# Optimization experiments

Hardware: AMD Instinct MI355X
Metric: run time of the kernel (lower is better)

Reference implementation:

```python
import jax, jax.numpy as jnp
import numpy as np

WIN = 7
NUM_HEADS = 4
HEAD_DIM = 32  # 128 / 4


def _relative_position_index(win=WIN):
    coords = np.stack(np.meshgrid(np.arange(win), np.arange(win), indexing='ij'))  # [2,w,w]
    coords = coords.reshape(2, -1)  # [2, w*w]
    rel = coords[:, :, None] - coords[:, None, :]  # [2, ws, ws]
    rel = rel.transpose(1, 2, 0)  # [ws, ws, 2]
    idx = (rel[..., 0] + win - 1) * (2 * win - 1) + (rel[..., 1] + win - 1)
    return jnp.asarray(idx, dtype=jnp.int32)  # [49, 49]


def setup_inputs() -> dict:
    key = jax.random.key(0)
    ks = jax.random.split(key, 6)
    B, S, D = 4096, WIN * WIN, 128
    nW = 64  # windows per image
    return {
        'hidden_states': jax.random.normal(ks[0], (B, S, D), dtype=jnp.float32),
        'attention_mask': jnp.zeros((nW, S, S), dtype=jnp.float32),
        'Wq': jax.random.normal(ks[1], (D, D), dtype=jnp.float32) * 0.02,
        'bq': jnp.zeros((D,), dtype=jnp.float32),
        'Wk': jax.random.normal(ks[2], (D, D), dtype=jnp.float32) * 0.02,
        'bk': jnp.zeros((D,), dtype=jnp.float32),
        'Wv': jax.random.normal(ks[3], (D, D), dtype=jnp.float32) * 0.02,
        'bv': jnp.zeros((D,), dtype=jnp.float32),
        'bias_table': jax.random.normal(ks[4], ((2 * WIN - 1) ** 2, NUM_HEADS), dtype=jnp.float32) * 0.02,
    }


def reference(hidden_states, attention_mask, Wq, bq, Wk, bk, Wv, bv, bias_table):
    B, S, D = hidden_states.shape
    H, Dh = NUM_HEADS, HEAD_DIM

    def heads(x):  # [B,S,D] -> [B,H,S,Dh]
        return x.reshape(B, S, H, Dh).transpose(0, 2, 1, 3)

    q = heads(hidden_states @ Wq + bq)
    k = heads(hidden_states @ Wk + bk)
    v = heads(hidden_states @ Wv + bv)

    scores = jnp.einsum('bhqd,bhkd->bhqk', q, k) / np.sqrt(Dh).astype(np.float32)

    idx = _relative_position_index()  # [S,S] int32 constant
    rel_bias = bias_table[idx]  # [S,S,H]
    scores = scores + rel_bias.transpose(2, 0, 1)[None]  # [B,H,S,S]

    nW = attention_mask.shape[0]
    scores = scores.reshape(B // nW, nW, H, S, S) + attention_mask[None, :, None]
    scores = scores.reshape(B, H, S, S)

    probs = jax.nn.softmax(scores, axis=-1)
    ctx = jnp.einsum('bhqk,bhkd->bhqd', probs, v)
    return ctx.transpose(0, 2, 1, 3).reshape(B, S, D)
```

## Files before the change

kernel.cpp:

```cpp
#include <hip/hip_runtime.h>
#include <hip/hip_bf16.h>

#define S49 49
#define D128 128
#define NH 4

typedef __attribute__((ext_vector_type(8))) short short8;
typedef __attribute__((ext_vector_type(4))) float f32x4;

__device__ __forceinline__ unsigned short f2b(float x){
  unsigned u = __builtin_bit_cast(unsigned, x);
  return (unsigned short)((u + 0x7fffu + ((u>>16)&1u)) >> 16);
}
__device__ __forceinline__ unsigned pk2(float a, float b){
  __hip_bfloat162 h = __float22bfloat162_rn(float2{a, b});
  unsigned u; __builtin_memcpy(&u, &h, 4);
  return u;
}
__device__ __forceinline__ int swz256i(int row, int col){
  return row*128 + ((((col>>3) ^ (row&15)) << 3) | (col&7));
}

__global__ void prep_wt(const float* __restrict__ Wq, const float* __restrict__ Wk,
                        const float* __restrict__ Wv, unsigned short* __restrict__ wt){
  int e = blockIdx.x*256 + threadIdx.x;
  if (e >= 3*128*128) return;
  int mat = e >> 14, rem = e & 16383, n = rem >> 7, k = rem & 127;
  const float* W = (mat==0) ? Wq : ((mat==1) ? Wk : Wv);
  wt[e] = f2b(W[k*128 + n]);
}

__global__ void prep_comb(const float* __restrict__ mask, const float* __restrict__ bt,
                          float4* __restrict__ comb4, int nW){
  int e = blockIdx.x*256 + threadIdx.x;
  if (e >= nW*NH*S49*16) return;
  int s = e & 15; int nt = s >> 2, lg = s & 3;
  int t = e >> 4;
  int i = t % S49; t /= S49;
  int h = t & (NH-1); int w = t / NH;
  const float* mrow = mask + ((size_t)w*S49 + i)*S49;
  int ri = i/7, ci = i - ri*7;
  const float L2E = 1.4426950408889634f;
  float v[4];
  #pragma unroll
  for (int r = 0; r < 4; ++r){
    int j = nt*16 + lg*4 + r;
    if (j < S49){
      int rj = j/7, cj = j - rj*7;
      int idx = (ri - rj + 6)*13 + (ci - cj + 6);
      v[r] = (mrow[j] + bt[idx*NH + h]) * L2E;
    } else v[r] = -1e30f;
  }
  float4 o; o.x = v[0]; o.y = v[1]; o.z = v[2]; o.w = v[3];
  comb4[e] = o;
}

__global__ __launch_bounds__(512, 6) void swin_attn(
    const float* __restrict__ hs,
    const float* __restrict__ bq, const float* __restrict__ bk,
    const float* __restrict__ bv,
    const float4* __restrict__ comb4,
    const unsigned short* __restrict__ wt, float* __restrict__ out, int nW){

  __shared__ __align__(16) unsigned short lds[26880];
  unsigned short* hs_s = lds;
  unsigned short* q_s  = lds + 6272;
  unsigned short* k_s  = lds + 12544;
  unsigned short* vt_s = lds + 18816;
  unsigned short* pext = lds + 25984;

  const int b = blockIdx.x;
  const int tid = threadIdx.x;
  const int wave = tid >> 6, lane = tid & 63;
  const int lg = lane >> 4, ln = lane & 15;
  unsigned short* pp = (wave < 7) ? (hs_s + wave*896) : pext;

  const float* hsb = hs + (size_t)b * (S49*D128);
  #pragma unroll
  for (int it = 0; it < 4; ++it) {
    int u = tid + it*512;
    if (u < S49*32) {
      int row = u >> 5, c = u & 31;
      float4 f = *(const float4*)(hsb + row*128 + c*4);
      uint2 o; o.x = pk2(f.x, f.y); o.y = pk2(f.z, f.w);
      *(uint2*)&hs_s[swz256i(row, c*4)] = o;
    }
  }
  if (tid < 128) {
    uint2 z2 = {0u,0u};
    *(uint2*)&vt_s[tid*56 + 48] = z2;
    *(uint2*)&vt_s[tid*56 + 52] = z2;
  }
  __syncthreads();

  const int w = b % nW;
  const int rt = wave & 3, hp = wave >> 2;
  const int mbw = (rt<3) ? rt*16 : 33;

  {
    const int ntb = wave*16;
    #pragma unroll 1
    for (int mat = 0; mat < 3; ++mat) {
      short8 a[4];
      #pragma unroll
      for (int ks = 0; ks < 4; ++ks)
        a[ks] = *(const short8*)&wt[(mat<<14) + (ntb+ln)*128 + ks*32 + lg*8];
      const float* bp = (mat==0) ? bq : ((mat==1) ? bk : bv);
      float4 bias = *(const float4*)&bp[ntb + 4*lg];
      #pragma unroll
      for (int mt = 0; mt < 4; ++mt) {
        const int mb = (mt<3) ? mt*16 : 33;
        short8 bh[4];
        #pragma unroll
        for (int ks = 0; ks < 4; ++ks)
          bh[ks] = *(const short8*)&hs_s[swz256i(mb+ln, ks*32 + lg*8)];
        f32x4 acc = {0.f,0.f,0.f,0.f};
        #pragma unroll
        for (int ks = 0; ks < 4; ++ks)
          acc = __builtin_amdgcn_mfma_f32_16x16x32_bf16(a[ks], bh[ks], acc, 0,0,0);
        const int m = mb + ln;
        const int nb = ntb + 4*lg;
        if (mat == 0) {
          uint2 o; o.x = pk2(acc[0]+bias.x, acc[1]+bias.y);
                   o.y = pk2(acc[2]+bias.z, acc[3]+bias.w);
          *(uint2*)&q_s[swz256i(m, nb)] = o;
        } else if (mat == 1) {
          uint2 o; o.x = pk2(acc[0]+bias.x, acc[1]+bias.y);
                   o.y = pk2(acc[2]+bias.z, acc[3]+bias.w);
          *(uint2*)&k_s[swz256i(m, nb)] = o;
        } else {
          vt_s[(nb+0)*56 + m] = f2b(acc[0]+bias.x);
          vt_s[(nb+1)*56 + m] = f2b(acc[1]+bias.y);
          vt_s[(nb+2)*56 + m] = f2b(acc[2]+bias.z);
          vt_s[(nb+3)*56 + m] = f2b(acc[3]+bias.w);
        }
      }
    }
  }
  __syncthreads();

  const float C1 = 0.17677669529663687f * 1.4426950408889634f;
  const short8 z8 = {0,0,0,0,0,0,0,0};

  #pragma unroll
  for (int hh = 0; hh < 2; ++hh) {
    const int h = hp*2 + hh;
    float4 cb[4];
    #pragma unroll
    for (int nt = 0; nt < 4; ++nt)
      cb[nt] = comb4[((size_t)((w*NH + h)*S49) + mbw + ln)*16 + nt*4 + lg];

    short8 aq = *(const short8*)&q_s[swz256i(mbw+ln, h*32 + lg*8)];
    short8 kb[4];
    #pragma unroll
    for (int nt = 0; nt < 4; ++nt)
      kb[nt] = *(const short8*)&k_s[swz256i(nt*16+ln, h*32 + lg*8)];
    if (ln != 0) kb[3] = z8;
    f32x4 st[4];
    __builtin_amdgcn_s_setprio(1);
    #pragma unroll
    for (int nt = 0; nt < 4; ++nt) {
      f32x4 z = {0.f,0.f,0.f,0.f};
      st[nt] = __builtin_amdgcn_mfma_f32_16x16x32_bf16(kb[nt], aq, z, 0,0,0);
    }
    __builtin_amdgcn_s_setprio(0);

    float e[4][4], psum[4];
    #pragma unroll
    for (int nt = 0; nt < 4; ++nt) {
      float cbv[4] = {cb[nt].x, cb[nt].y, cb[nt].z, cb[nt].w};
      #pragma unroll
      for (int r = 0; r < 4; ++r)
        e[nt][r] = __builtin_amdgcn_exp2f(fmaf(st[nt][r], C1, cbv[r]));
      psum[nt] = (e[nt][0] + e[nt][1]) + (e[nt][2] + e[nt][3]);
    }
    float sum = (psum[0] + psum[1]) + (psum[2] + psum[3]);
    sum += __shfl_xor(sum, 16, 64);
    sum += __shfl_xor(sum, 32, 64);
    const float inv = __builtin_amdgcn_rcpf(sum);

    #pragma unroll
    for (int nt = 0; nt < 4; ++nt) {
      #pragma unroll
      for (int rp = 0; rp < 2; ++rp) {
        if (nt < 3 || lg < 2) {
          unsigned u = pk2(e[nt][2*rp]*inv, e[nt][2*rp+1]*inv);
          *(unsigned*)&pp[ln*56 + nt*16 + lg*4 + 2*rp] = u;
        }
      }
    }

    short8 ap0 = *(const short8*)&pp[ln*56 + lg*8];
    short8 ap1 = z8;
    if (lg < 3) ap1 = *(const short8*)&pp[ln*56 + 32 + lg*8];
    #pragma unroll
    for (int nt = 0; nt < 2; ++nt) {
      const int vr = h*32 + nt*16 + ln;
      short8 bv0 = *(const short8*)&vt_s[vr*56 + lg*8];
      short8 bv1 = z8;
      if (lg < 3) bv1 = *(const short8*)&vt_s[vr*56 + 32 + lg*8];
      f32x4 acc = {0.f,0.f,0.f,0.f};
      __builtin_amdgcn_s_setprio(1);
      acc = __builtin_amdgcn_mfma_f32_16x16x32_bf16(ap0, bv0, acc, 0,0,0);
      acc = __builtin_amdgcn_mfma_f32_16x16x32_bf16(ap1, bv1, acc, 0,0,0);
      __builtin_amdgcn_s_setprio(0);
      const int mr = mbw + 4*lg;
      #pragma unroll
      for (int r = 0; r < 4; ++r)
        out[((size_t)b*S49 + mr + r)*D128 + vr] = acc[r];
    }
  }
}

extern "C" void kernel_launch(void* const* d_in, const int* in_sizes, int n_in,
                              void* d_out, int out_size, void* d_ws, size_t ws_size,
                              hipStream_t stream){
  const float* hs  = (const float*)d_in[0];
  const float* msk = (const float*)d_in[1];
  const float* Wq  = (const float*)d_in[2];
  const float* bq  = (const float*)d_in[3];
  const float* Wk  = (const float*)d_in[4];
  const float* bk  = (const float*)d_in[5];
  const float* Wv  = (const float*)d_in[6];
  const float* bv  = (const float*)d_in[7];
  const float* bt  = (const float*)d_in[8];
  unsigned short* wt = (unsigned short*)d_ws;
  float4* comb4 = (float4*)((char*)d_ws + 98304);
  float* out = (float*)d_out;
  const int B  = in_sizes[0] / (S49*D128);
  const int nW = in_sizes[1] / (S49*S49);
  prep_wt<<<dim3((3*128*128 + 255)/256), dim3(256), 0, stream>>>(Wq, Wk, Wv, wt);
  prep_comb<<<dim3((nW*NH*S49*16 + 255)/256), dim3(256), 0, stream>>>(msk, bt, comb4, nW);
  swin_attn<<<dim3(B), dim3(512), 0, stream>>>(hs, bq, bk, bv, comb4, wt, out, nW);
}
```

Measured before the change: 109.2 us.

## Permute key order so softmax probabilities feed the PV MFMA from registers

Keys are reordered through a lane-to-row mapping, krow, and the combined mask/bias table is permuted to match. The QK^T MFMA output then already sits in the A-operand layout the PV MFMA expects, so the probabilities are packed in registers instead of written to LDS and read back. This removes an LDS store/load round trip and shrinks shared memory. The V-transpose stride also changes from 56 to 58 to cut bank conflicts. The risks are that 16-byte LDS reads at a 58-element stride are not 16-byte aligned, and that padded key rows now read past k_s into other LDS data, relying only on the -1e30 bias to mask them.

```diff
diff --git a/kernel.cpp b/kernel.cpp
--- a/kernel.cpp
+++ b/kernel.cpp
@@ -4,8 +4,10 @@
 #define S49 49
 #define D128 128
 #define NH 4
+#define VTS 58
 
 typedef __attribute__((ext_vector_type(8))) short short8;
+typedef __attribute__((ext_vector_type(4))) unsigned uint4v;
 typedef __attribute__((ext_vector_type(4))) float f32x4;
 
 __device__ __forceinline__ unsigned short f2b(float x){
@@ -19,6 +21,9 @@
 }
 __device__ __forceinline__ int swz256i(int row, int col){
   return row*128 + ((((col>>3) ^ (row&15)) << 3) | (col&7));
+}
+__device__ __forceinline__ int krow(int nt, int ln){
+  return 8*(ln>>2) + (ln&3) + 4*(nt&1) + 32*(nt>>1);
 }
 
 __global__ void prep_wt(const float* __restrict__ Wq, const float* __restrict__ Wk,
@@ -44,7 +49,7 @@
   float v[4];
   #pragma unroll
   for (int r = 0; r < 4; ++r){
-    int j = nt*16 + lg*4 + r;
+    int j = 8*lg + 4*(nt&1) + 32*(nt>>1) + r;
     if (j < S49){
       int rj = j/7, cj = j - rj*7;
       int idx = (ri - rj + 6)*13 + (ci - cj + 6);
@@ -62,18 +67,16 @@
     const float4* __restrict__ comb4,
     const unsigned short* __restrict__ wt, float* __restrict__ out, int nW){
 
-  __shared__ __align__(16) unsigned short lds[26880];
+  __shared__ __align__(16) unsigned short lds[26240];
   unsigned short* hs_s = lds;
   unsigned short* q_s  = lds + 6272;
   unsigned short* k_s  = lds + 12544;
   unsigned short* vt_s = lds + 18816;
-  unsigned short* pext = lds + 25984;
 
   const int b = blockIdx.x;
   const int tid = threadIdx.x;
   const int wave = tid >> 6, lane = tid & 63;
   const int lg = lane >> 4, ln = lane & 15;
-  unsigned short* pp = (wave < 7) ? (hs_s + wave*896) : pext;
 
   const float* hsb = hs + (size_t)b * (S49*D128);
   #pragma unroll
@@ -86,10 +89,13 @@
       *(uint2*)&hs_s[swz256i(row, c*4)] = o;
     }
   }
-  if (tid < 128) {
-    uint2 z2 = {0u,0u};
-    *(uint2*)&vt_s[tid*56 + 48] = z2;
-    *(uint2*)&vt_s[tid*56 + 52] = z2;
+  #pragma unroll
+  for (int it = 0; it < 2; ++it) {
+    int u = tid + it*512;
+    if (u < 128*5) {
+      int row = u/5, cc = 48 + 2*(u - row*5);
+      *(unsigned*)&vt_s[row*VTS + cc] = 0u;
+    }
   }
   __syncthreads();
 
@@ -129,10 +135,10 @@
                    o.y = pk2(acc[2]+bias.z, acc[3]+bias.w);
           *(uint2*)&k_s[swz256i(m, nb)] = o;
         } else {
-          vt_s[(nb+0)*56 + m] = f2b(acc[0]+bias.x);
-          vt_s[(nb+1)*56 + m] = f2b(acc[1]+bias.y);
-          vt_s[(nb+2)*56 + m] = f2b(acc[2]+bias.z);
-          vt_s[(nb+3)*56 + m] = f2b(acc[3]+bias.w);
+          vt_s[(nb+0)*VTS + m] = f2b(acc[0]+bias.x);
+          vt_s[(nb+1)*VTS + m] = f2b(acc[1]+bias.y);
+          vt_s[(nb+2)*VTS + m] = f2b(acc[2]+bias.z);
+          vt_s[(nb+3)*VTS + m] = f2b(acc[3]+bias.w);
         }
       }
     }
@@ -154,8 +160,7 @@
     short8 kb[4];
     #pragma unroll
     for (int nt = 0; nt < 4; ++nt)
-      kb[nt] = *(const short8*)&k_s[swz256i(nt*16+ln, h*32 + lg*8)];
-    if (ln != 0) kb[3] = z8;
+      kb[nt] = *(const short8*)&k_s[swz256i(krow(nt, ln), h*32 + lg*8)];
     f32x4 st[4];
     __builtin_amdgcn_s_setprio(1);
     #pragma unroll
@@ -179,26 +184,24 @@
     sum += __shfl_xor(sum, 32, 64);
     const float inv = __builtin_amdgcn_rcpf(sum);
 
-    #pragma unroll
-    for (int nt = 0; nt < 4; ++nt) {
-      #pragma unroll
-      for (int rp = 0; rp < 2; ++rp) {
-        if (nt < 3 || lg < 2) {
-          unsigned u = pk2(e[nt][2*rp]*inv, e[nt][2*rp+1]*inv);
-          *(unsigned*)&pp[ln*56 + nt*16 + lg*4 + 2*rp] = u;
-        }
-      }
-    }
-
-    short8 ap0 = *(const short8*)&pp[ln*56 + lg*8];
-    short8 ap1 = z8;
-    if (lg < 3) ap1 = *(const short8*)&pp[ln*56 + 32 + lg*8];
+    uint4v u0, u1;
+    u0.x = pk2(e[0][0]*inv, e[0][1]*inv);
+    u0.y = pk2(e[0][2]*inv, e[0][3]*inv);
+    u0.z = pk2(e[1][0]*inv, e[1][1]*inv);
+    u0.w = pk2(e[1][2]*inv, e[1][3]*inv);
+    u1.x = pk2(e[2][0]*inv, e[2][1]*inv);
+    u1.y = pk2(e[2][2]*inv, e[2][3]*inv);
+    u1.z = pk2(e[3][0]*inv, e[3][1]*inv);
+    u1.w = pk2(e[3][2]*inv, e[3][3]*inv);
+    short8 ap0 = __builtin_bit_cast(short8, u0);
+    short8 ap1 = __builtin_bit_cast(short8, u1);
+
     #pragma unroll
     for (int nt = 0; nt < 2; ++nt) {
       const int vr = h*32 + nt*16 + ln;
-      short8 bv0 = *(const short8*)&vt_s[vr*56 + lg*8];
+      short8 bv0 = *(const short8*)&vt_s[vr*VTS + lg*8];
       short8 bv1 = z8;
-      if (lg < 3) bv1 = *(const short8*)&vt_s[vr*56 + 32 + lg*8];
+      if (lg < 3) bv1 = *(const short8*)&vt_s[vr*VTS + 32 + lg*8];
       f32x4 acc = {0.f,0.f,0.f,0.f};
       __builtin_amdgcn_s_setprio(1);
       acc = __builtin_amdgcn_mfma_f32_16x16x32_bf16(ap0, bv0, acc, 0,0,0);
```

After: 110.0 us. No clear change (+0.7%).
